# Kernel optimization log

Measured on AMD Instinct MI355X. Metric: run time of the kernel, lower is better.

## Reference

```python
import jax, jax.numpy as jnp
import numpy as np
import math

D_MODEL = 96
D_STATE = 16
D_CONV = 3
EXPAND = 2
D_INNER = EXPAND * D_MODEL          # 192
DT_RANK = math.ceil(D_MODEL / 16)   # 6
B_SZ, H_SZ, W_SZ = 2, 56, 56


def setup_inputs() -> dict:
    key = jax.random.key(0)
    ks = jax.random.split(key, 10)
    x = jax.random.normal(ks[0], (B_SZ, H_SZ, W_SZ, D_MODEL), jnp.float32)
    W_in = jax.random.normal(ks[1], (D_MODEL, 2 * D_INNER), jnp.float32) * 0.02
    conv_w = jax.random.normal(ks[2], (D_CONV, D_CONV, 1, D_INNER), jnp.float32) * 0.1
    conv_b = jax.random.normal(ks[3], (D_INNER,), jnp.float32) * 0.02
    W_xproj = jax.random.normal(ks[4], (D_INNER, DT_RANK + 2 * D_STATE), jnp.float32) * 0.02
    dt_std = DT_RANK ** -0.5
    W_dt = jax.random.uniform(ks[5], (DT_RANK, D_INNER), jnp.float32, -dt_std, dt_std)
    # dt_proj bias init: inverse-softplus of dt ~ LogUniform(dt_min, dt_max)
    dt_min, dt_max = 1e-3, 1e-1
    dt = jnp.exp(jax.random.uniform(ks[6], (D_INNER,), jnp.float32)
                 * (math.log(dt_max) - math.log(dt_min)) + math.log(dt_min))
    dt = jnp.clip(dt, 1e-4, None)
    b_dt = dt + jnp.log(-jnp.expm1(-dt))
    # A_log initialized to broadcast arange(1..d_state) (as in the source, no log taken)
    A_log = jnp.tile(jnp.arange(1, D_STATE + 1, dtype=jnp.float32)[None, :], (D_INNER, 1))
    D_skip = jnp.ones((D_INNER,), jnp.float32)
    W_out = jax.random.normal(ks[7], (D_INNER, D_MODEL), jnp.float32) * 0.02
    return {"x": x, "W_in": W_in, "conv_w": conv_w, "conv_b": conv_b,
            "W_xproj": W_xproj, "W_dt": W_dt, "b_dt": b_dt,
            "A_log": A_log, "D_skip": D_skip, "W_out": W_out}


def _selective_scan(xs, dt, A, Bm, Cm, D_skip):
    """Canonical Mamba selective scan.
    xs, dt: (G, L, C); Bm, Cm: (G, L, N); A: (C, N); D_skip: (C,).
    h_l = exp(dt_l * A) * h_{l-1} + dt_l * B_l * x_l ;  y_l = <h_l, C_l> + D * x_l
    """
    dA = jnp.exp(dt[..., None] * A)                              # (G,L,C,N)
    dBx = dt[..., None] * Bm[:, :, None, :] * xs[..., None]      # (G,L,C,N)

    def step(h, inp):
        dA_l, dBx_l, C_l = inp                                   # (G,C,N),(G,C,N),(G,N)
        h = dA_l * h + dBx_l
        y = jnp.einsum('gcn,gn->gc', h, C_l)
        return h, y

    G, L, C = xs.shape
    h0 = jnp.zeros((G, C, D_STATE), xs.dtype)
    _, ys = jax.lax.scan(step, h0, (jnp.moveaxis(dA, 1, 0),
                                    jnp.moveaxis(dBx, 1, 0),
                                    jnp.moveaxis(Cm, 1, 0)))
    ys = jnp.moveaxis(ys, 0, 1)                                  # (G,L,C)
    return ys + D_skip * xs


def reference(x, W_in, conv_w, conv_b, W_xproj, W_dt, b_dt, A_log, D_skip, W_out):
    B, H, W, _ = x.shape  # H == W required (source sums transposed scans directly)
    xz = x @ W_in                                                # (B,H,W,2*d_inner)
    xm, z = jnp.split(xz, 2, axis=-1)
    pad = (D_CONV - 1) // 2
    xm = jax.lax.conv_general_dilated(
        xm, conv_w, (1, 1), [(pad, pad), (pad, pad)],
        dimension_numbers=('NHWC', 'HWIO', 'NHWC'),
        feature_group_count=D_INNER) + conv_b                    # depthwise conv
    # 4 scan directions
    xt = jnp.swapaxes(xm, 1, 2)
    xs4 = jnp.stack([xm, jnp.flip(xm, 2), xt, jnp.flip(xt, 1)], 0)  # (4,B,H,W,C)
    G, L = 4 * B, H * W
    xs = xs4.reshape(G, L, D_INNER)
    x_dbl = xs @ W_xproj                                          # (G,L,dt_rank+2N)
    dtr, Bm, Cm = jnp.split(x_dbl, [DT_RANK, DT_RANK + D_STATE], axis=-1)
    dt = jax.nn.softplus(dtr @ W_dt + b_dt)                       # (G,L,d_inner)
    A = -jnp.exp(A_log)                                           # (d_inner, N)
    ys = _selective_scan(xs, dt, A, Bm, Cm, D_skip)               # (G,L,d_inner)
    y = ys.reshape(4, B, H, W, D_INNER).sum(0)                    # sum 4 directions
    y = jax.nn.silu(z) * y
    return y @ W_out                                              # (B,H,W,d_model)
```

## Files before the change

kernel.cpp:

```cpp
#include <hip/hip_runtime.h>
#include <math.h>

#define NPIX 6272
#define LVAL 3136
#define CIN 192
#define NST 16
#define HW 56

__device__ __forceinline__ float softplusf(float v) {
    return (v > 20.0f) ? v : log1pf(expf(v));
}

__device__ __forceinline__ void dir_geom(int d, int b, int& si, int& sj, int& off) {
    if (d == 0)      { si = HW;  sj = 1;   off = b * LVAL; }
    else if (d == 1) { si = HW;  sj = -1;  off = b * LVAL + (HW - 1); }
    else if (d == 2) { si = 1;   sj = HW;  off = b * LVAL; }
    else             { si = -1;  sj = HW;  off = b * LVAL + (HW - 1); }
}

__global__ __launch_bounds__(384) void k_inproj(
    const float* __restrict__ x, const float* __restrict__ W_in,
    float* __restrict__ xm, float* __restrict__ z)
{
    __shared__ __align__(16) float xs[96][20];
    const int p0 = blockIdx.x * 16;
    const int t = threadIdx.x;
    for (int e = t; e < 16 * 96; e += 384) {
        int p = e / 96, kk = e % 96;
        xs[kk][p] = x[p0 * 96 + e];
    }
    __syncthreads();
    float acc[16];
#pragma unroll
    for (int p = 0; p < 16; ++p) acc[p] = 0.f;
    for (int k = 0; k < 96; ++k) {
        float w = W_in[k * 384 + t];
        float4 x0 = *(const float4*)&xs[k][0];
        float4 x1 = *(const float4*)&xs[k][4];
        float4 x2 = *(const float4*)&xs[k][8];
        float4 x3 = *(const float4*)&xs[k][12];
        acc[0]  = fmaf(x0.x, w, acc[0]);  acc[1]  = fmaf(x0.y, w, acc[1]);
        acc[2]  = fmaf(x0.z, w, acc[2]);  acc[3]  = fmaf(x0.w, w, acc[3]);
        acc[4]  = fmaf(x1.x, w, acc[4]);  acc[5]  = fmaf(x1.y, w, acc[5]);
        acc[6]  = fmaf(x1.z, w, acc[6]);  acc[7]  = fmaf(x1.w, w, acc[7]);
        acc[8]  = fmaf(x2.x, w, acc[8]);  acc[9]  = fmaf(x2.y, w, acc[9]);
        acc[10] = fmaf(x2.z, w, acc[10]); acc[11] = fmaf(x2.w, w, acc[11]);
        acc[12] = fmaf(x3.x, w, acc[12]); acc[13] = fmaf(x3.y, w, acc[13]);
        acc[14] = fmaf(x3.z, w, acc[14]); acc[15] = fmaf(x3.w, w, acc[15]);
    }
#pragma unroll
    for (int p = 0; p < 16; ++p) {
        int pix = p0 + p;
        if (t < 192) xm[pix * CIN + t] = acc[p];
        else         z[pix * CIN + (t - 192)] = acc[p];
    }
}

__global__ __launch_bounds__(256) void k_conv(
    const float* __restrict__ xm, const float* __restrict__ cw,
    const float* __restrict__ cb, float* __restrict__ xcv)
{
    int e = blockIdx.x * 256 + threadIdx.x;
    if (e >= NPIX * (CIN / 4)) return;
    int cq = (e % (CIN / 4)) * 4;
    int pix = e / (CIN / 4);
    int w = pix % HW;
    int rest = pix / HW;
    int h = rest % HW;
    int b = rest / HW;
    float4 acc = *(const float4*)&cb[cq];
#pragma unroll
    for (int ky = 0; ky < 3; ++ky) {
        int hh = h + ky - 1;
        if (hh < 0 || hh >= HW) continue;
#pragma unroll
        for (int kx = 0; kx < 3; ++kx) {
            int ww = w + kx - 1;
            if (ww < 0 || ww >= HW) continue;
            float4 xv = *(const float4*)&xm[((b * HW + hh) * HW + ww) * CIN + cq];
            float4 wv = *(const float4*)&cw[(ky * 3 + kx) * CIN + cq];
            acc.x = fmaf(xv.x, wv.x, acc.x);
            acc.y = fmaf(xv.y, wv.y, acc.y);
            acc.z = fmaf(xv.z, wv.z, acc.z);
            acc.w = fmaf(xv.w, wv.w, acc.w);
        }
    }
    *(float4*)&xcv[pix * CIN + cq] = acc;
}

__global__ __launch_bounds__(512) void k_xproj_dt(
    const float* __restrict__ xcv, const float* __restrict__ W_xproj,
    const float* __restrict__ W_dt, const float* __restrict__ b_dt,
    float* __restrict__ Bp, float* __restrict__ Cp, float2* __restrict__ dtx2)
{
    __shared__ __align__(16) float xs[192][28];
    __shared__ float part[2][24][40];
    __shared__ float dtr_lds[24][8];
    const int p0 = blockIdx.x * 24;
    const int t = threadIdx.x;
    for (int e = t; e < 24 * 192; e += 512) {
        int p = e / 192, kk = e % 192;
        int pix = p0 + p;
        xs[kk][p] = (pix < NPIX) ? xcv[pix * CIN + kk] : 0.f;
    }
    __syncthreads();
    const int th = t & 255;
    const int kh = t >> 8;
    const int j  = th % 40;
    const int pq = th / 40;
    if (pq < 6) {
        const int jc = (j < 38) ? j : 37;
        float a0 = 0.f, a1 = 0.f, a2 = 0.f, a3 = 0.f;
        const int k0 = kh * 96;
        for (int k = k0; k < k0 + 96; ++k) {
            float w = W_xproj[k * 38 + jc];
            float4 xv = *(const float4*)&xs[k][pq * 4];
            a0 = fmaf(xv.x, w, a0); a1 = fmaf(xv.y, w, a1);
            a2 = fmaf(xv.z, w, a2); a3 = fmaf(xv.w, w, a3);
        }
        part[kh][pq * 4 + 0][j] = a0;
        part[kh][pq * 4 + 1][j] = a1;
        part[kh][pq * 4 + 2][j] = a2;
        part[kh][pq * 4 + 3][j] = a3;
    }
    __syncthreads();
    if (kh == 0 && pq < 6 && j < 38) {
#pragma unroll
        for (int q = 0; q < 4; ++q) {
            int p = pq * 4 + q;
            float r = part[0][p][j] + part[1][p][j];
            int pix = p0 + p;
            if (j < 6) dtr_lds[p][j] = r;
            if (pix < NPIX) {
                if (j < 6)       ;
                else if (j < 22) Bp[pix * NST + (j - 6)] = r;
                else             Cp[pix * NST + (j - 22)] = r;
            }
        }
    }
    __syncthreads();
    for (int e = t; e < 24 * 192; e += 512) {
        int p = e / 192, c = e % 192;
        int pix = p0 + p;
        if (pix >= NPIX) continue;
        float v = b_dt[c];
#pragma unroll
        for (int r = 0; r < 6; ++r)
            v = fmaf(dtr_lds[p][r], W_dt[r * CIN + c], v);
        dtx2[(size_t)pix * CIN + c] = make_float2(softplusf(v), xs[c][p]);
    }
}

template<int CHUNK>
__global__ __launch_bounds__(384) void k_scan_p1(
    const float2* __restrict__ dtx2, const float* __restrict__ Bp,
    const float* __restrict__ A_log,
    float* __restrict__ Pbuf, float* __restrict__ qbuf)
{
    constexpr int CPR = HW / CHUNK;
    __shared__ __align__(16) float Bs[CHUNK * NST];
    const int g = blockIdx.y;
    const int k = blockIdx.x;
    const int t = threadIdx.x;
    const int wv = t >> 6;
    const int lane = t & 63;
    const int cl = lane & 31, nh = lane >> 5;
    const int c = wv * 32 + cl;
    const int n0 = nh * 8;
    const int d = g >> 1, b = g & 1;
    int si, sj, off;
    dir_geom(d, b, si, sj, off);
    const int base = off + (k / CPR) * si + ((k % CPR) * CHUNK) * sj;

    for (int e = t; e < CHUNK * NST; e += 384) {
        int jj = e >> 4, n = e & 15;
        Bs[e] = Bp[(base + jj * sj) * NST + n];
    }

    const float LOG2E = 1.4426950408889634f;
    float a2[8];
    {
        const float4* Ar = (const float4*)(A_log + c * NST + n0);
#pragma unroll
        for (int q = 0; q < 2; ++q) {
            float4 v = Ar[q];
            a2[q*4+0] = -expf(v.x) * LOG2E;
            a2[q*4+1] = -expf(v.y) * LOG2E;
            a2[q*4+2] = -expf(v.z) * LOG2E;
            a2[q*4+3] = -expf(v.w) * LOG2E;
        }
    }
    __syncthreads();

    float h[8];
#pragma unroll
    for (int i = 0; i < 8; ++i) h[i] = 0.f;
    float Sdt = 0.f;

    float2 dv = dtx2[(size_t)base * CIN + c];
    for (int jj = 0; jj < CHUNK; ++jj) {
        float dt_c = dv.x, x_c = dv.y;
        int jn = (jj + 1 < CHUNK) ? jj + 1 : jj;
        dv = dtx2[(size_t)(base + jn * sj) * CIN + c];
        float dtx = dt_c * x_c;
        Sdt += dt_c;
        float Bv[8];
        {
            const float4* Brow = (const float4*)(Bs + jj * NST + n0);
            float4 t0 = Brow[0], t1 = Brow[1];
            Bv[0]=t0.x; Bv[1]=t0.y; Bv[2]=t0.z; Bv[3]=t0.w;
            Bv[4]=t1.x; Bv[5]=t1.y; Bv[6]=t1.z; Bv[7]=t1.w;
        }
#pragma unroll
        for (int i = 0; i < 8; ++i) {
            float dA = exp2f(dt_c * a2[i]);
            h[i] = fmaf(dA, h[i], dtx * Bv[i]);
        }
    }
    float P[8];
#pragma unroll
    for (int i = 0; i < 8; ++i) P[i] = exp2f(a2[i] * Sdt);

    float4* Pd = (float4*)(Pbuf + ((size_t)(k * 8 + g) * CIN + c) * NST + n0);
    float4* qd = (float4*)(qbuf + ((size_t)(k * 8 + g) * CIN + c) * NST + n0);
    Pd[0] = make_float4(P[0], P[1], P[2], P[3]);
    Pd[1] = make_float4(P[4], P[5], P[6], P[7]);
    qd[0] = make_float4(h[0], h[1], h[2], h[3]);
    qd[1] = make_float4(h[4], h[5], h[6], h[7]);
}

__global__ __launch_bounds__(256) void k_scan_fix(
    const float* __restrict__ Pbuf, float* __restrict__ qbuf, int nch)
{
    const int g = blockIdx.y;
    const int lo = blockIdx.x * 256 + threadIdx.x;
    const size_t stride = (size_t)8 * CIN * NST;
    size_t idx  = (size_t)g * CIN * NST + lo;
    size_t pidx = idx;
    float Pr[8], qr[8];
#pragma unroll
    for (int i = 0; i < 8; ++i) { Pr[i] = Pbuf[pidx]; qr[i] = qbuf[pidx]; pidx += stride; }
    float h = 0.f;
    for (int k = 0; k < nch; k += 8) {
        float Pn[8], qn[8];
        if (k + 8 < nch) {
#pragma unroll
            for (int i = 0; i < 8; ++i) {
                Pn[i] = Pbuf[pidx + (size_t)i * stride];
                qn[i] = qbuf[pidx + (size_t)i * stride];
            }
        } else {
#pragma unroll
            for (int i = 0; i < 8; ++i) { Pn[i] = 0.f; qn[i] = 0.f; }
        }
#pragma unroll
        for (int i = 0; i < 8; ++i) {
            qbuf[idx] = h;
            h = fmaf(Pr[i], h, qr[i]);
            idx += stride;
        }
#pragma unroll
        for (int i = 0; i < 8; ++i) { Pr[i] = Pn[i]; qr[i] = qn[i]; }
        pidx += (size_t)8 * stride;
    }
}

template<int CHUNK>
__global__ __launch_bounds__(384) void k_scan_p2(
    const float2* __restrict__ dtx2, const float* __restrict__ Bp,
    const float* __restrict__ Cp, const float* __restrict__ A_log,
    const float* __restrict__ D_skip,
    const float* __restrict__ qbuf, float* __restrict__ Y4)
{
    constexpr int CPR = HW / CHUNK;
    __shared__ __align__(16) float Bs[CHUNK * NST];
    __shared__ __align__(16) float Cs[CHUNK * NST];
    const int g = blockIdx.y;
    const int k = blockIdx.x;
    const int t = threadIdx.x;
    const int wv = t >> 6;
    const int lane = t & 63;
    const int cl = lane & 31, nh = lane >> 5;
    const int c = wv * 32 + cl;
    const int n0 = nh * 8;
    const int d = g >> 1, b = g & 1;
    int si, sj, off;
    dir_geom(d, b, si, sj, off);
    const int base = off + (k / CPR) * si + ((k % CPR) * CHUNK) * sj;

    for (int e = t; e < CHUNK * NST; e += 384) {
        int jj = e >> 4, n = e & 15;
        int pa = (base + jj * sj) * NST + n;
        Bs[e] = Bp[pa];
        Cs[e] = Cp[pa];
    }

    const float LOG2E = 1.4426950408889634f;
    float a2[8];
    {
        const float4* Ar = (const float4*)(A_log + c * NST + n0);
#pragma unroll
        for (int q = 0; q < 2; ++q) {
            float4 v = Ar[q];
            a2[q*4+0] = -expf(v.x) * LOG2E;
            a2[q*4+1] = -expf(v.y) * LOG2E;
            a2[q*4+2] = -expf(v.z) * LOG2E;
            a2[q*4+3] = -expf(v.w) * LOG2E;
        }
    }
    const float Dc = D_skip[c];

    float h[8];
    {
        const float4* qd = (const float4*)(qbuf + ((size_t)(k * 8 + g) * CIN + c) * NST + n0);
        float4 v0 = qd[0], v1 = qd[1];
        h[0]=v0.x; h[1]=v0.y; h[2]=v0.z; h[3]=v0.w;
        h[4]=v1.x; h[5]=v1.y; h[6]=v1.z; h[7]=v1.w;
    }
    __syncthreads();

    float* yo = Y4 + ((size_t)d * NPIX + (size_t)b * LVAL + (size_t)k * CHUNK) * CIN;

    float2 dv = dtx2[(size_t)base * CIN + c];
    for (int jj = 0; jj < CHUNK; ++jj) {
        float dt_c = dv.x, x_c = dv.y;
        int jn = (jj + 1 < CHUNK) ? jj + 1 : jj;
        dv = dtx2[(size_t)(base + jn * sj) * CIN + c];
        float dtx = dt_c * x_c;
        float Bv[8], Cv[8];
        {
            const float4* Brow = (const float4*)(Bs + jj * NST + n0);
            const float4* Crow = (const float4*)(Cs + jj * NST + n0);
            float4 t0 = Brow[0], t1 = Brow[1];
            float4 u0 = Crow[0], u1 = Crow[1];
            Bv[0]=t0.x; Bv[1]=t0.y; Bv[2]=t0.z; Bv[3]=t0.w;
            Bv[4]=t1.x; Bv[5]=t1.y; Bv[6]=t1.z; Bv[7]=t1.w;
            Cv[0]=u0.x; Cv[1]=u0.y; Cv[2]=u0.z; Cv[3]=u0.w;
            Cv[4]=u1.x; Cv[5]=u1.y; Cv[6]=u1.z; Cv[7]=u1.w;
        }
        float yc0 = 0.f, yc1 = 0.f;
#pragma unroll
        for (int i = 0; i < 8; i += 2) {
            float dA0 = exp2f(dt_c * a2[i]);
            float dA1 = exp2f(dt_c * a2[i+1]);
            h[i]   = fmaf(dA0, h[i],   dtx * Bv[i]);
            h[i+1] = fmaf(dA1, h[i+1], dtx * Bv[i+1]);
            yc0 = fmaf(h[i],   Cv[i],   yc0);
            yc1 = fmaf(h[i+1], Cv[i+1], yc1);
        }
        float yc = yc0 + yc1;
        yc += __shfl_xor(yc, 32, 64);
        if (nh == 0)
            yo[jj * CIN + c] = fmaf(Dc, x_c, yc);
    }
}

__global__ __launch_bounds__(384) void k_gateout(
    const float* __restrict__ Y4, const float* __restrict__ z,
    const float* __restrict__ W_out, float* __restrict__ out)
{
    __shared__ __align__(16) float xs[192][20];
    const int p0 = blockIdx.x * 16;
    const int t = threadIdx.x;
    const size_t NP = (size_t)NPIX * CIN;
    for (int e = t; e < 16 * 192; e += 384) {
        int p = e / 192, c = e % 192;
        size_t idx = (size_t)(p0 + p) * CIN + c;
        float s = Y4[idx] + Y4[idx + NP] + Y4[idx + 2 * NP] + Y4[idx + 3 * NP];
        float zz = z[idx];
        float sig = 1.f / (1.f + expf(-zz));
        xs[c][p] = zz * sig * s;
    }
    __syncthreads();
    const int j  = t % 96;
    const int ph = t / 96;
    float acc[4] = {0.f, 0.f, 0.f, 0.f};
    for (int k = 0; k < 192; ++k) {
        float w = W_out[k * 96 + j];
        float4 xv = *(const float4*)&xs[k][ph * 4];
        acc[0] = fmaf(xv.x, w, acc[0]); acc[1] = fmaf(xv.y, w, acc[1]);
        acc[2] = fmaf(xv.z, w, acc[2]); acc[3] = fmaf(xv.w, w, acc[3]);
    }
#pragma unroll
    for (int p = 0; p < 4; ++p)
        out[(p0 + ph * 4 + p) * 96 + j] = acc[p];
}

template<int CHUNK>
static void launch_scan(const float2* dtx2, const float* Bp, const float* Cp,
                        const float* A_log, const float* D_skip,
                        float* Pbuf, float* qbuf, float* Y4, hipStream_t stream)
{
    const int nch = LVAL / CHUNK;
    k_scan_p1<CHUNK><<<dim3(nch, 8), 384, 0, stream>>>(dtx2, Bp, A_log, Pbuf, qbuf);
    k_scan_fix<<<dim3(12, 8), 256, 0, stream>>>(Pbuf, qbuf, nch);
    k_scan_p2<CHUNK><<<dim3(nch, 8), 384, 0, stream>>>(dtx2, Bp, Cp, A_log, D_skip, qbuf, Y4);
}

extern "C" void kernel_launch(void* const* d_in, const int* in_sizes, int n_in,
                              void* d_out, int out_size, void* d_ws, size_t ws_size,
                              hipStream_t stream) {
    const float* x      = (const float*)d_in[0];
    const float* W_in   = (const float*)d_in[1];
    const float* conv_w = (const float*)d_in[2];
    const float* conv_b = (const float*)d_in[3];
    const float* W_xproj= (const float*)d_in[4];
    const float* W_dt   = (const float*)d_in[5];
    const float* b_dt   = (const float*)d_in[6];
    const float* A_log  = (const float*)d_in[7];
    const float* D_skip = (const float*)d_in[8];
    const float* W_out  = (const float*)d_in[9];
    float* out = (float*)d_out;

    float* ws   = (float*)d_ws;
    float* xm   = ws;
    float* z    = xm  + NPIX * CIN;
    float* xcv  = z   + NPIX * CIN;
    float2* dtx2= (float2*)(xcv + NPIX * CIN);
    float* Bp   = (float*)(dtx2 + (size_t)NPIX * CIN);
    float* Cp   = Bp  + NPIX * NST;
    float* Y4   = Cp  + NPIX * NST;
    float* Pbuf = Y4  + (size_t)4 * NPIX * CIN;

    const size_t base_fl = 11038720;
    const size_t ws_fl = ws_size / 4;
    int chunk;
    if (ws_fl >= base_fl + (size_t)2 * 112 * 24576) chunk = 28;
    else                                            chunk = 56;
    float* qbuf = Pbuf + (size_t)(LVAL / chunk) * 8 * CIN * NST;

    k_inproj  <<<NPIX / 16, 384, 0, stream>>>(x, W_in, xm, z);
    k_conv    <<<(NPIX * (CIN / 4)) / 256, 256, 0, stream>>>(xm, conv_w, conv_b, xcv);
    k_xproj_dt<<<(NPIX + 23) / 24, 512, 0, stream>>>(xcv, W_xproj, W_dt, b_dt, Bp, Cp, dtx2);
    if (chunk == 28) launch_scan<28>(dtx2, Bp, Cp, A_log, D_skip, Pbuf, qbuf, Y4, stream);
    else             launch_scan<56>(dtx2, Bp, Cp, A_log, D_skip, Pbuf, qbuf, Y4, stream);
    k_gateout <<<NPIX / 16, 384, 0, stream>>>(Y4, z, W_out, out);
}
```

Measured before the change: 197.0 us.

## Fuse depthwise conv into xproj and use single-pass decoupled-lookback scan

```diff
diff --git a/kernel.cpp b/kernel.cpp
--- a/kernel.cpp
+++ b/kernel.cpp
@@ -6,6 +6,11 @@
 #define CIN 192
 #define NST 16
 #define HW 56
+
+#define KSTEPS 112
+#define KCH 28
+#define NCHAIN 16
+#define NFLAGS (NCHAIN * KCH)
 
 __device__ __forceinline__ float softplusf(float v) {
     return (v > 20.0f) ? v : log1pf(expf(v));
@@ -56,52 +61,46 @@
     }
 }
 
-__global__ __launch_bounds__(256) void k_conv(
+__global__ __launch_bounds__(512) void k_xproj_dt(
     const float* __restrict__ xm, const float* __restrict__ cw,
-    const float* __restrict__ cb, float* __restrict__ xcv)
-{
-    int e = blockIdx.x * 256 + threadIdx.x;
-    if (e >= NPIX * (CIN / 4)) return;
-    int cq = (e % (CIN / 4)) * 4;
-    int pix = e / (CIN / 4);
-    int w = pix % HW;
-    int rest = pix / HW;
-    int h = rest % HW;
-    int b = rest / HW;
-    float4 acc = *(const float4*)&cb[cq];
-#pragma unroll
-    for (int ky = 0; ky < 3; ++ky) {
-        int hh = h + ky - 1;
-        if (hh < 0 || hh >= HW) continue;
-#pragma unroll
-        for (int kx = 0; kx < 3; ++kx) {
-            int ww = w + kx - 1;
-            if (ww < 0 || ww >= HW) continue;
-            float4 xv = *(const float4*)&xm[((b * HW + hh) * HW + ww) * CIN + cq];
-            float4 wv = *(const float4*)&cw[(ky * 3 + kx) * CIN + cq];
-            acc.x = fmaf(xv.x, wv.x, acc.x);
-            acc.y = fmaf(xv.y, wv.y, acc.y);
-            acc.z = fmaf(xv.z, wv.z, acc.z);
-            acc.w = fmaf(xv.w, wv.w, acc.w);
-        }
-    }
-    *(float4*)&xcv[pix * CIN + cq] = acc;
-}
-
-__global__ __launch_bounds__(512) void k_xproj_dt(
-    const float* __restrict__ xcv, const float* __restrict__ W_xproj,
+    const float* __restrict__ cb,
+    const float* __restrict__ W_xproj,
     const float* __restrict__ W_dt, const float* __restrict__ b_dt,
-    float* __restrict__ Bp, float* __restrict__ Cp, float2* __restrict__ dtx2)
+    float* __restrict__ Bp, float* __restrict__ Cp, float2* __restrict__ dtx2,
+    int* __restrict__ flags_ticket)
 {
     __shared__ __align__(16) float xs[192][28];
     __shared__ float part[2][24][40];
     __shared__ float dtr_lds[24][8];
     const int p0 = blockIdx.x * 24;
     const int t = threadIdx.x;
+    if (blockIdx.x == 0) {
+        for (int e = t; e < NFLAGS + 1; e += 512) flags_ticket[e] = 0;
+    }
     for (int e = t; e < 24 * 192; e += 512) {
         int p = e / 192, kk = e % 192;
         int pix = p0 + p;
-        xs[kk][p] = (pix < NPIX) ? xcv[pix * CIN + kk] : 0.f;
+        float v = 0.f;
+        if (pix < NPIX) {
+            int w = pix % HW;
+            int rest = pix / HW;
+            int h = rest % HW;
+            int b = rest / HW;
+            v = cb[kk];
+#pragma unroll
+            for (int ky = 0; ky < 3; ++ky) {
+                int hh = h + ky - 1;
+                if (hh < 0 || hh >= HW) continue;
+#pragma unroll
+                for (int kx = 0; kx < 3; ++kx) {
+                    int ww = w + kx - 1;
+                    if (ww < 0 || ww >= HW) continue;
+                    v = fmaf(xm[((b * HW + hh) * HW + ww) * CIN + kk],
+                             cw[(ky * 3 + kx) * CIN + kk], v);
+                }
+            }
+        }
+        xs[kk][p] = v;
     }
     __syncthreads();
     const int th = t & 255;
@@ -151,207 +150,147 @@
     }
 }
 
-template<int CHUNK>
-__global__ __launch_bounds__(384) void k_scan_p1(
+__global__ __launch_bounds__(384) void k_scan_lb(
     const float2* __restrict__ dtx2, const float* __restrict__ Bp,
-    const float* __restrict__ A_log,
-    float* __restrict__ Pbuf, float* __restrict__ qbuf)
+    const float* __restrict__ Cp, const float* __restrict__ A_log,
+    const float* __restrict__ D_skip,
+    float* __restrict__ carry, int* __restrict__ flags, int* __restrict__ ticket,
+    float* __restrict__ Y4)
 {
-    constexpr int CPR = HW / CHUNK;
-    __shared__ __align__(16) float Bs[CHUNK * NST];
-    const int g = blockIdx.y;
-    const int k = blockIdx.x;
+    __shared__ __align__(16) float Bs[KSTEPS * NST];
+    __shared__ __align__(16) float Cs[KSTEPS * NST];
+    __shared__ int vk_s;
     const int t = threadIdx.x;
-    const int wv = t >> 6;
-    const int lane = t & 63;
-    const int cl = lane & 31, nh = lane >> 5;
-    const int c = wv * 32 + cl;
-    const int n0 = nh * 8;
+    if (t == 0) vk_s = atomicAdd(ticket, 1);
+    __syncthreads();
+    const int vid = vk_s;
+    const int chain = vid & (NCHAIN - 1);
+    const int myk   = vid >> 4;
+    const int g  = chain >> 1;
+    const int ch = chain & 1;
+    const int wv = t >> 6, lane = t & 63;
+    const int cl = lane & 15, nh = lane >> 4;
+    const int c    = ch * 96 + wv * 16 + cl;
+    const int cloc = wv * 16 + cl;
+    const int n0 = nh * 4;
     const int d = g >> 1, b = g & 1;
     int si, sj, off;
     dir_geom(d, b, si, sj, off);
-    const int base = off + (k / CPR) * si + ((k % CPR) * CHUNK) * sj;
-
-    for (int e = t; e < CHUNK * NST; e += 384) {
+    const int r0 = myk * 2;
+
+    for (int e = t; e < KSTEPS * NST; e += 384) {
         int jj = e >> 4, n = e & 15;
-        Bs[e] = Bp[(base + jj * sj) * NST + n];
+        int rr = (jj >= 56) ? 1 : 0;
+        int j  = jj - rr * 56;
+        int pix = off + (r0 + rr) * si + j * sj;
+        Bs[e] = Bp[pix * NST + n];
+        Cs[e] = Cp[pix * NST + n];
     }
 
     const float LOG2E = 1.4426950408889634f;
-    float a2[8];
+    float a2[4];
     {
-        const float4* Ar = (const float4*)(A_log + c * NST + n0);
-#pragma unroll
-        for (int q = 0; q < 2; ++q) {
-            float4 v = Ar[q];
-            a2[q*4+0] = -expf(v.x) * LOG2E;
-            a2[q*4+1] = -expf(v.y) * LOG2E;
-            a2[q*4+2] = -expf(v.z) * LOG2E;
-            a2[q*4+3] = -expf(v.w) * LOG2E;
-        }
-    }
-    __syncthreads();
-
-    float h[8];
-#pragma unroll
-    for (int i = 0; i < 8; ++i) h[i] = 0.f;
+        float4 v = *(const float4*)(A_log + c * NST + n0);
+        a2[0] = -expf(v.x) * LOG2E;
+        a2[1] = -expf(v.y) * LOG2E;
+        a2[2] = -expf(v.z) * LOG2E;
+        a2[3] = -expf(v.w) * LOG2E;
+    }
+    __syncthreads();
+
+    const ptrdiff_t dstep = (ptrdiff_t)sj * CIN;
+
+    float h[4] = {0.f, 0.f, 0.f, 0.f};
     float Sdt = 0.f;
-
-    float2 dv = dtx2[(size_t)base * CIN + c];
-    for (int jj = 0; jj < CHUNK; ++jj) {
-        float dt_c = dv.x, x_c = dv.y;
-        int jn = (jj + 1 < CHUNK) ? jj + 1 : jj;
-        dv = dtx2[(size_t)(base + jn * sj) * CIN + c];
-        float dtx = dt_c * x_c;
-        Sdt += dt_c;
-        float Bv[8];
-        {
-            const float4* Brow = (const float4*)(Bs + jj * NST + n0);
-            float4 t0 = Brow[0], t1 = Brow[1];
-            Bv[0]=t0.x; Bv[1]=t0.y; Bv[2]=t0.z; Bv[3]=t0.w;
-            Bv[4]=t1.x; Bv[5]=t1.y; Bv[6]=t1.z; Bv[7]=t1.w;
-        }
-#pragma unroll
-        for (int i = 0; i < 8; ++i) {
-            float dA = exp2f(dt_c * a2[i]);
-            h[i] = fmaf(dA, h[i], dtx * Bv[i]);
-        }
-    }
-    float P[8];
-#pragma unroll
-    for (int i = 0; i < 8; ++i) P[i] = exp2f(a2[i] * Sdt);
-
-    float4* Pd = (float4*)(Pbuf + ((size_t)(k * 8 + g) * CIN + c) * NST + n0);
-    float4* qd = (float4*)(qbuf + ((size_t)(k * 8 + g) * CIN + c) * NST + n0);
-    Pd[0] = make_float4(P[0], P[1], P[2], P[3]);
-    Pd[1] = make_float4(P[4], P[5], P[6], P[7]);
-    qd[0] = make_float4(h[0], h[1], h[2], h[3]);
-    qd[1] = make_float4(h[4], h[5], h[6], h[7]);
-}
-
-__global__ __launch_bounds__(256) void k_scan_fix(
-    const float* __restrict__ Pbuf, float* __restrict__ qbuf, int nch)
-{
-    const int g = blockIdx.y;
-    const int lo = blockIdx.x * 256 + threadIdx.x;
-    const size_t stride = (size_t)8 * CIN * NST;
-    size_t idx  = (size_t)g * CIN * NST + lo;
-    size_t pidx = idx;
-    float Pr[8], qr[8];
-#pragma unroll
-    for (int i = 0; i < 8; ++i) { Pr[i] = Pbuf[pidx]; qr[i] = qbuf[pidx]; pidx += stride; }
-    float h = 0.f;
-    for (int k = 0; k < nch; k += 8) {
-        float Pn[8], qn[8];
-        if (k + 8 < nch) {
-#pragma unroll
-            for (int i = 0; i < 8; ++i) {
-                Pn[i] = Pbuf[pidx + (size_t)i * stride];
-                qn[i] = qbuf[pidx + (size_t)i * stride];
-            }
-        } else {
-#pragma unroll
-            for (int i = 0; i < 8; ++i) { Pn[i] = 0.f; qn[i] = 0.f; }
-        }
-#pragma unroll
-        for (int i = 0; i < 8; ++i) {
-            qbuf[idx] = h;
-            h = fmaf(Pr[i], h, qr[i]);
-            idx += stride;
-        }
-#pragma unroll
-        for (int i = 0; i < 8; ++i) { Pr[i] = Pn[i]; qr[i] = qn[i]; }
-        pidx += (size_t)8 * stride;
-    }
-}
-
-template<int CHUNK>
-__global__ __launch_bounds__(384) void k_scan_p2(
-    const float2* __restrict__ dtx2, const float* __restrict__ Bp,
-    const float* __restrict__ Cp, const float* __restrict__ A_log,
-    const float* __restrict__ D_skip,
-    const float* __restrict__ qbuf, float* __restrict__ Y4)
-{
-    constexpr int CPR = HW / CHUNK;
-    __shared__ __align__(16) float Bs[CHUNK * NST];
-    __shared__ __align__(16) float Cs[CHUNK * NST];
-    const int g = blockIdx.y;
-    const int k = blockIdx.x;
-    const int t = threadIdx.x;
-    const int wv = t >> 6;
-    const int lane = t & 63;
-    const int cl = lane & 31, nh = lane >> 5;
-    const int c = wv * 32 + cl;
-    const int n0 = nh * 8;
-    const int d = g >> 1, b = g & 1;
-    int si, sj, off;
-    dir_geom(d, b, si, sj, off);
-    const int base = off + (k / CPR) * si + ((k % CPR) * CHUNK) * sj;
-
-    for (int e = t; e < CHUNK * NST; e += 384) {
-        int jj = e >> 4, n = e & 15;
-        int pa = (base + jj * sj) * NST + n;
-        Bs[e] = Bp[pa];
-        Cs[e] = Cp[pa];
-    }
-
-    const float LOG2E = 1.4426950408889634f;
-    float a2[8];
-    {
-        const float4* Ar = (const float4*)(A_log + c * NST + n0);
-#pragma unroll
-        for (int q = 0; q < 2; ++q) {
-            float4 v = Ar[q];
-            a2[q*4+0] = -expf(v.x) * LOG2E;
-            a2[q*4+1] = -expf(v.y) * LOG2E;
-            a2[q*4+2] = -expf(v.z) * LOG2E;
-            a2[q*4+3] = -expf(v.w) * LOG2E;
-        }
-    }
+    for (int rr = 0; rr < 2; ++rr) {
+        const float2* dp = dtx2 + (size_t)(off + (r0 + rr) * si) * CIN + c;
+        const float* Brow = Bs + rr * 56 * NST;
+#pragma unroll 4
+        for (int j2 = 0; j2 < 56; ++j2) {
+            float2 dv = dp[(ptrdiff_t)j2 * dstep];
+            float dt_c = dv.x, x_c = dv.y;
+            float dtx = dt_c * x_c;
+            Sdt += dt_c;
+            float4 bq = *(const float4*)(Brow + j2 * NST + n0);
+            float Bv[4] = {bq.x, bq.y, bq.z, bq.w};
+#pragma unroll
+            for (int i = 0; i < 4; ++i) {
+                float dA = exp2f(dt_c * a2[i]);
+                h[i] = fmaf(dA, h[i], dtx * Bv[i]);
+            }
+        }
+    }
+    float P[4];
+#pragma unroll
+    for (int i = 0; i < 4; ++i) P[i] = exp2f(a2[i] * Sdt);
+
+    const int slot = chain * KCH + myk;
+    float cin[4] = {0.f, 0.f, 0.f, 0.f};
+    if (myk > 0) {
+        if (t == 0) {
+            long long spins = 0;
+            while (__hip_atomic_load(&flags[slot - 1], __ATOMIC_ACQUIRE,
+                                     __HIP_MEMORY_SCOPE_AGENT) == 0) {
+                if (++spins > 200000000LL) break;
+            }
+        }
+        __syncthreads();
+        const float* cp = carry + (size_t)(slot - 1) * 1536 + cloc * NST + n0;
+#pragma unroll
+        for (int i = 0; i < 4; ++i)
+            cin[i] = __hip_atomic_load(cp + i, __ATOMIC_RELAXED,
+                                       __HIP_MEMORY_SCOPE_AGENT);
+    }
+    if (myk < KCH - 1) {
+        float* co = carry + (size_t)slot * 1536 + cloc * NST + n0;
+#pragma unroll
+        for (int i = 0; i < 4; ++i) {
+            float inc = fmaf(P[i], cin[i], h[i]);
+            __hip_atomic_store(co + i, inc, __ATOMIC_RELAXED,
+                               __HIP_MEMORY_SCOPE_AGENT);
+        }
+        __syncthreads();
+        if (t == 0) {
+            __threadfence();
+            __hip_atomic_store(&flags[slot], 1, __ATOMIC_RELEASE,
+                               __HIP_MEMORY_SCOPE_AGENT);
+        }
+    }
+
     const float Dc = D_skip[c];
-
-    float h[8];
-    {
-        const float4* qd = (const float4*)(qbuf + ((size_t)(k * 8 + g) * CIN + c) * NST + n0);
-        float4 v0 = qd[0], v1 = qd[1];
-        h[0]=v0.x; h[1]=v0.y; h[2]=v0.z; h[3]=v0.w;
-        h[4]=v1.x; h[5]=v1.y; h[6]=v1.z; h[7]=v1.w;
-    }
-    __syncthreads();
-
-    float* yo = Y4 + ((size_t)d * NPIX + (size_t)b * LVAL + (size_t)k * CHUNK) * CIN;
-
-    float2 dv = dtx2[(size_t)base * CIN + c];
-    for (int jj = 0; jj < CHUNK; ++jj) {
-        float dt_c = dv.x, x_c = dv.y;
-        int jn = (jj + 1 < CHUNK) ? jj + 1 : jj;
-        dv = dtx2[(size_t)(base + jn * sj) * CIN + c];
-        float dtx = dt_c * x_c;
-        float Bv[8], Cv[8];
-        {
-            const float4* Brow = (const float4*)(Bs + jj * NST + n0);
-            const float4* Crow = (const float4*)(Cs + jj * NST + n0);
-            float4 t0 = Brow[0], t1 = Brow[1];
-            float4 u0 = Crow[0], u1 = Crow[1];
-            Bv[0]=t0.x; Bv[1]=t0.y; Bv[2]=t0.z; Bv[3]=t0.w;
-            Bv[4]=t1.x; Bv[5]=t1.y; Bv[6]=t1.z; Bv[7]=t1.w;
-            Cv[0]=u0.x; Cv[1]=u0.y; Cv[2]=u0.z; Cv[3]=u0.w;
-            Cv[4]=u1.x; Cv[5]=u1.y; Cv[6]=u1.z; Cv[7]=u1.w;
-        }
-        float yc0 = 0.f, yc1 = 0.f;
-#pragma unroll
-        for (int i = 0; i < 8; i += 2) {
-            float dA0 = exp2f(dt_c * a2[i]);
-            float dA1 = exp2f(dt_c * a2[i+1]);
-            h[i]   = fmaf(dA0, h[i],   dtx * Bv[i]);
-            h[i+1] = fmaf(dA1, h[i+1], dtx * Bv[i+1]);
-            yc0 = fmaf(h[i],   Cv[i],   yc0);
-            yc1 = fmaf(h[i+1], Cv[i+1], yc1);
-        }
-        float yc = yc0 + yc1;
-        yc += __shfl_xor(yc, 32, 64);
-        if (nh == 0)
-            yo[jj * CIN + c] = fmaf(Dc, x_c, yc);
+#pragma unroll
+    for (int i = 0; i < 4; ++i) h[i] = cin[i];
+    for (int rr = 0; rr < 2; ++rr) {
+        const float2* dp = dtx2 + (size_t)(off + (r0 + rr) * si) * CIN + c;
+        const float* Brow = Bs + rr * 56 * NST;
+        const float* Crow = Cs + rr * 56 * NST;
+        float* yo = Y4 + ((size_t)d * NPIX + (size_t)b * LVAL
+                          + (size_t)(r0 + rr) * 56) * CIN;
+#pragma unroll 4
+        for (int j2 = 0; j2 < 56; ++j2) {
+            float2 dv = dp[(ptrdiff_t)j2 * dstep];
+            float dt_c = dv.x, x_c = dv.y;
+            float dtx = dt_c * x_c;
+            float4 bq = *(const float4*)(Brow + j2 * NST + n0);
+            float4 uq = *(const float4*)(Crow + j2 * NST + n0);
+            float Bv[4] = {bq.x, bq.y, bq.z, bq.w};
+            float Cv[4] = {uq.x, uq.y, uq.z, uq.w};
+            float yc0 = 0.f, yc1 = 0.f;
+#pragma unroll
+            for (int i = 0; i < 4; i += 2) {
+                float dA0 = exp2f(dt_c * a2[i]);
+                float dA1 = exp2f(dt_c * a2[i+1]);
+                h[i]   = fmaf(dA0, h[i],   dtx * Bv[i]);
+                h[i+1] = fmaf(dA1, h[i+1], dtx * Bv[i+1]);
+                yc0 = fmaf(h[i],   Cv[i],   yc0);
+                yc1 = fmaf(h[i+1], Cv[i+1], yc1);
+            }
+            float yc = yc0 + yc1;
+            yc += __shfl_xor(yc, 16, 64);
+            yc += __shfl_xor(yc, 32, 64);
+            if (nh == 0)
+                yo[j2 * CIN + c] = fmaf(Dc, x_c, yc);
+        }
     }
 }
 
@@ -386,17 +325,6 @@
         out[(p0 + ph * 4 + p) * 96 + j] = acc[p];
 }
 
-template<int CHUNK>
-static void launch_scan(const float2* dtx2, const float* Bp, const float* Cp,
-                        const float* A_log, const float* D_skip,
-                        float* Pbuf, float* qbuf, float* Y4, hipStream_t stream)
-{
-    const int nch = LVAL / CHUNK;
-    k_scan_p1<CHUNK><<<dim3(nch, 8), 384, 0, stream>>>(dtx2, Bp, A_log, Pbuf, qbuf);
-    k_scan_fix<<<dim3(12, 8), 256, 0, stream>>>(Pbuf, qbuf, nch);
-    k_scan_p2<CHUNK><<<dim3(nch, 8), 384, 0, stream>>>(dtx2, Bp, Cp, A_log, D_skip, qbuf, Y4);
-}
-
 extern "C" void kernel_launch(void* const* d_in, const int* in_sizes, int n_in,
                               void* d_out, int out_size, void* d_ws, size_t ws_size,
                               hipStream_t stream) {
@@ -420,19 +348,15 @@
     float* Bp   = (float*)(dtx2 + (size_t)NPIX * CIN);
     float* Cp   = Bp  + NPIX * NST;
     float* Y4   = Cp  + NPIX * NST;
-    float* Pbuf = Y4  + (size_t)4 * NPIX * CIN;
-
-    const size_t base_fl = 11038720;
-    const size_t ws_fl = ws_size / 4;
-    int chunk;
-    if (ws_fl >= base_fl + (size_t)2 * 112 * 24576) chunk = 28;
-    else                                            chunk = 56;
-    float* qbuf = Pbuf + (size_t)(LVAL / chunk) * 8 * CIN * NST;
+    float* carry= Y4  + (size_t)4 * NPIX * CIN;
+    int*  flags = (int*)(carry + (size_t)NCHAIN * KCH * 1536);
+    int*  ticket= flags + NFLAGS;
 
     k_inproj  <<<NPIX / 16, 384, 0, stream>>>(x, W_in, xm, z);
-    k_conv    <<<(NPIX * (CIN / 4)) / 256, 256, 0, stream>>>(xm, conv_w, conv_b, xcv);
-    k_xproj_dt<<<(NPIX + 23) / 24, 512, 0, stream>>>(xcv, W_xproj, W_dt, b_dt, Bp, Cp, dtx2);
-    if (chunk == 28) launch_scan<28>(dtx2, Bp, Cp, A_log, D_skip, Pbuf, qbuf, Y4, stream);
-    else             launch_scan<56>(dtx2, Bp, Cp, A_log, D_skip, Pbuf, qbuf, Y4, stream);
+    k_xproj_dt<<<(NPIX + 23) / 24, 512, 0, stream>>>(xm, conv_w, conv_b,
+                                                     W_xproj, W_dt, b_dt,
+                                                     Bp, Cp, dtx2, flags);
+    k_scan_lb <<<NCHAIN * KCH, 384, 0, stream>>>(dtx2, Bp, Cp, A_log, D_skip,
+                                                 carry, flags, ticket, Y4);
     k_gateout <<<NPIX / 16, 384, 0, stream>>>(Y4, z, W_out, out);
 }
```

Result: slower. 511.7 us (+159.8%).
